# Kernel tuning notes

Measured on AMD Instinct MI355X. Metric: run time of the kernel, lower is better.

## Reference

```python
import jax, jax.numpy as jnp
import numpy as np

TOPK_RATIOS = (0.67, 0.75, 0.8)


def setup_inputs() -> dict:
    key = jax.random.key(0)
    k0, k1, k2 = jax.random.split(key, 3)
    B, L, S, H, E, D = 4, 2048, 2048, 8, 64, 64
    queries = jax.random.normal(k0, (B, L, H, E), dtype=jnp.float32)
    keys = jax.random.normal(k1, (B, S, H, E), dtype=jnp.float32)
    values = jax.random.normal(k2, (B, S, H, D), dtype=jnp.float32)
    attn_weights = jnp.ones((len(TOPK_RATIOS),), dtype=jnp.float32)  # nn.Parameter(ones)
    attn_mask = jnp.zeros((1,), dtype=bool)  # unused by the module
    return {"queries": queries, "keys": keys, "values": values,
            "attn_weights": attn_weights, "attn_mask": attn_mask}


def reference(queries, keys, values, attn_weights, attn_mask):
    # queries: [B,L,H,E], keys: [B,S,H,E], values: [B,S,H,D]
    B, L, H, E = queries.shape
    S = keys.shape[1]
    scale = 1.0 / np.sqrt(E)  # self.scale is None -> 1/sqrt(E)
    scores = jnp.einsum('blhe,bshe->bhls', queries, keys) * scale  # [B,H,L,S]
    out = jnp.zeros(queries.shape[:3] + (values.shape[-1],), dtype=scores.dtype)
    for i, ratio in enumerate(TOPK_RATIOS):
        k = int(S * ratio)
        topv = jax.lax.top_k(scores, k)[0]            # sorted descending
        kth = topv[..., -1:]                           # k-th largest per row
        # mask==0 -> -inf, then softmax over S (ties at threshold are measure-zero)
        masked = jnp.where(scores >= kth, scores, -jnp.inf)
        attn = jax.nn.softmax(masked, axis=-1)         # dropout = identity (eval)
        out = out + jnp.einsum('bhls,bshd->blhd', attn, values) * attn_weights[i]
    return out
```

## Files before the change

### kernel.cpp

```cpp
#include <hip/hip_runtime.h>
#include <hip/hip_fp16.h>

typedef _Float16 f16x8 __attribute__((ext_vector_type(8)));
typedef float f32x4 __attribute__((ext_vector_type(4)));

#define KSEL0 1372u
#define KSEL1 1536u
#define KSEL2 1638u
#define WSC 16.0f
#define QS   0.1803368801f
#define CSH2 11.5416222f

__device__ __forceinline__ unsigned ou16_inv(unsigned ou) {
  return (ou & 0x8000u) ? (ou ^ 0x8000u) : (ou ^ 0xFFFFu);
}
__device__ __forceinline__ unsigned ou16x2(unsigned uu) {
  return uu ^ 0x80008000u ^ (((uu >> 15) & 0x00010001u) * 0x7FFFu);
}
__device__ __forceinline__ unsigned pk2(float a, float b) {
  auto h = __builtin_amdgcn_cvt_pkrtz(a, b);
  return __builtin_bit_cast(unsigned, h);
}
__device__ __forceinline__ unsigned shflx(unsigned v, int m) {
  return (unsigned)__shfl_xor((int)v, m, 64);
}
__device__ __forceinline__ float h2f(unsigned bits16) {
  return __half2float(__ushort_as_half((unsigned short)bits16));
}

__device__ __forceinline__ unsigned suffix64(unsigned s4, int lane) {
  unsigned p = s4;
  #pragma unroll
  for (int off = 1; off < 64; off <<= 1) {
    int sl = lane + off;
    unsigned t = (unsigned)__shfl((int)p, sl < 64 ? sl : lane, 64);
    p += (sl < 64) ? t : 0u;
  }
  return p;
}
__device__ __forceinline__ unsigned pick_digit(unsigned tail, unsigned hx, unsigned hy,
                                               unsigned hz, unsigned hw_, unsigned k, int lane) {
  unsigned s4 = hx + hy + hz + hw_;
  unsigned a3 = tail - s4;
  unsigned a2 = a3 + hw_;
  unsigned a1 = a2 + hz;
  unsigned a0 = a1 + hy;
  int d = -1; unsigned nk = 0;
  if (a3 < k && a3 + hw_ >= k)      { d = 4*lane+3; nk = k - a3; }
  else if (a2 < k && a2 + hz >= k)  { d = 4*lane+2; nk = k - a2; }
  else if (a1 < k && a1 + hy >= k)  { d = 4*lane+1; nk = k - a1; }
  else if (a0 < k && a0 + hx >= k)  { d = 4*lane+0; nk = k - a0; }
  unsigned long long mb = __ballot(d >= 0);
  int src = __ffsll(mb) - 1;
  unsigned pack = ((unsigned)d << 16) | nk;
  return (unsigned)__shfl((int)pack, src, 64);
}

extern "C" __global__ __launch_bounds__(256)
void prep_kv(const float* __restrict__ K, const float* __restrict__ V,
             unsigned short* __restrict__ Kh, unsigned short* __restrict__ Vt) {
  if (blockIdx.x < 2048) {
    int idx = blockIdx.x * 256 + threadIdx.x;
    int ec = idx & 7;
    int s  = (idx >> 3) & 2047;
    int bh = idx >> 14;
    int b = bh >> 3, h = bh & 7;
    const float* src = K + (((size_t)b * 2048 + s) * 8 + h) * 64 + ec * 8;
    float4 a = *(const float4*)src;
    float4 c = *(const float4*)(src + 4);
    uint4 val = { pk2(a.x, a.y), pk2(a.z, a.w), pk2(c.x, c.y), pk2(c.z, c.w) };
    *(uint4*)(Kh + (size_t)idx * 8) = val;
  } else {
    const int bid  = blockIdx.x - 2048;
    const int tid  = threadIdx.x;
    const int w    = tid >> 6;
    const int lane = tid & 63;
    const int u_   = lane >> 4;
    const int dq   = (lane >> 2) & 3;
    const int r_   = lane & 3;
    const unsigned selv = (lane & 1) ? 0x03020706u : 0x05040100u;

    int bh = bid >> 4;
    int s0 = (bid & 15) * 128;
    int b = bh >> 3, h = bh & 7;
    const float* Vb = V + ((size_t)b * 2048 * 8 + h) * 64;
    unsigned short* Vo = Vt + (size_t)bh * 64 * 2048;

    #pragma unroll
    for (int sp = 0; sp < 2; ++sp) {
      #pragma unroll
      for (int p = 0; p < 4; ++p) {
        int sl = w * 32 + sp * 16 + u_ * 4;
        int sg = s0 + sl + r_;
        int d0 = p * 16 + dq * 4;
        float4 f = *(const float4*)(Vb + (size_t)sg * 512 + d0);
        unsigned lo = pk2(f.x, f.y), hi = pk2(f.z, f.w);
        unsigned tlo = shflx(lo, 1), thi = shflx(hi, 1);
        lo = __builtin_amdgcn_perm(tlo, lo, selv);
        hi = __builtin_amdgcn_perm(thi, hi, selv);
        unsigned t2lo = shflx(lo, 2), t2hi = shflx(hi, 2);
        unsigned Aw = (lane & 2) ? t2hi : lo;
        unsigned Bw = (lane & 2) ? hi   : t2lo;
        int d = d0 + r_;
        uint2 wv = {Aw, Bw};
        *(uint2*)(Vo + (size_t)d * 2048 + s0 + sl) = wv;
      }
    }
  }
}

extern "C" __global__ __launch_bounds__(512, 4)
void nma_kernel(const float* __restrict__ Q, const unsigned short* __restrict__ Kh,
                const unsigned short* __restrict__ Vt, const float* __restrict__ AW,
                float* __restrict__ Out)
{
  __shared__ __align__(16) char lds[81920];
  unsigned* work = (unsigned*)(lds + 65536);

  const int tid  = threadIdx.x;
  const int w    = tid >> 6;
  const int lane = tid & 63;
  const int g    = lane >> 4;
  const int lx   = lane & 15;

  int bid = blockIdx.x;
  int lb  = (bid & 7) * 512 + (bid >> 3);
  int bh  = lb >> 7;
  int b   = bh >> 3, hh = bh & 7;
  int l0  = (lb & 127) << 4;

  const float* Qb = Q + (((size_t)b * 2048 + l0) * 8 + hh) * 64;
  const unsigned short* Khb = Kh + (size_t)bh * 2048 * 64;
  const unsigned short* Vtb = Vt + (size_t)bh * 64 * 2048;

  {
    uint4 z4 = {0u,0u,0u,0u};
    uint4* p = (uint4*)work;
    p[tid] = z4;
    p[tid + 512] = z4;
  }

  union FU { f16x8 v; unsigned u[4]; };
  FU qa0, qa1;
  {
    const float* qp = Qb + (size_t)lx * 512 + g * 8;
    float4 a = *(const float4*)(qp);
    float4 c = *(const float4*)(qp + 4);
    qa0.u[0] = pk2(a.x*QS, a.y*QS); qa0.u[1] = pk2(a.z*QS, a.w*QS);
    qa0.u[2] = pk2(c.x*QS, c.y*QS); qa0.u[3] = pk2(c.z*QS, c.w*QS);
    a = *(const float4*)(qp + 32);
    c = *(const float4*)(qp + 36);
    qa1.u[0] = pk2(a.x*QS, a.y*QS); qa1.u[1] = pk2(a.z*QS, a.w*QS);
    qa1.u[2] = pk2(c.x*QS, c.y*QS); qa1.u[3] = pk2(c.z*QS, c.w*QS);
  }
  __syncthreads();

  const unsigned swl = ((unsigned)(lx & 7)) << 4;
  const unsigned rot = ((unsigned)lx) << 2;
  const unsigned hinc = (g < 2) ? 1u : 0x10000u;
  unsigned* hq = work + lx * 256;
  #pragma unroll 4
  for (int t = 0; t < 16; ++t) {
    int s0 = (t * 8 + w) * 16;
    const unsigned short* kp = Khb + (size_t)(s0 + lx) * 64 + g * 8;
    f16x8 kb0 = *(const f16x8*)(kp);
    f16x8 kb1 = *(const f16x8*)(kp + 32);
    f32x4 acc = {0.f, 0.f, 0.f, 0.f};
    acc = __builtin_amdgcn_mfma_f32_16x16x32_f16(kb0, qa0.v, acc, 0, 0, 0);
    acc = __builtin_amdgcn_mfma_f32_16x16x32_f16(kb1, qa1.v, acc, 0, 0, 0);
    unsigned u0 = pk2(acc[0], acc[1]);
    unsigned u1 = pk2(acc[2], acc[3]);
    uint2 wv = {u0, u1};
    *(uint2*)(lds + lx * 4096 + (((unsigned)(s0 * 2 + g * 8)) ^ swl)) = wv;
    unsigned o20 = ou16x2(u0), o21 = ou16x2(u1);
    atomicAdd(&hq[(((o20 >>  8) & 255u) + rot) & 255u], hinc);
    atomicAdd(&hq[(( o20 >> 24)         + rot) & 255u], hinc);
    atomicAdd(&hq[(((o21 >>  8) & 255u) + rot) & 255u], hinc);
    atomicAdd(&hq[(( o21 >> 24)         + rot) & 255u], hinc);
  }
  __syncthreads();

  const float aw0 = AW[0], aw1 = AW[1], aw2 = AW[2];

  unsigned d0a[2], d1a[2], d2a[2], k0a[2], k1a[2], k2a[2];
  #pragma unroll 2
  for (int rr = 0; rr < 2; ++rr) {
    int q = 2 * w + rr;
    uint4 hr = ((const uint4*)(work + q * 256))[(lane + q) & 63];
    unsigned hbx = (hr.x & 0xFFFFu) + (hr.x >> 16);
    unsigned hby = (hr.y & 0xFFFFu) + (hr.y >> 16);
    unsigned hbz = (hr.z & 0xFFFFu) + (hr.z >> 16);
    unsigned hbw = (hr.w & 0xFFFFu) + (hr.w >> 16);
    unsigned tail = suffix64(hbx + hby + hbz + hbw, lane);
    unsigned p0 = pick_digit(tail, hbx, hby, hbz, hbw, KSEL0, lane);
    unsigned p1 = pick_digit(tail, hbx, hby, hbz, hbw, KSEL1, lane);
    unsigned p2 = pick_digit(tail, hbx, hby, hbz, hbw, KSEL2, lane);
    d0a[rr] = p0 >> 16; k0a[rr] = p0 & 0xFFFFu;
    d1a[rr] = p1 >> 16; k1a[rr] = p1 & 0xFFFFu;
    d2a[rr] = p2 >> 16; k2a[rr] = p2 & 0xFFFFu;
  }

  unsigned* hw2 = work + w * 512;
  #pragma unroll 1
  for (int rr = 0; rr < 2; ++rr) {
    int q = 2 * w + rr;
    const unsigned swq = ((unsigned)(q & 7)) << 4;
    char* rowp = lds + q * 4096;
    for (int i = lane; i < 512; i += 64) hw2[i] = 0u;
    unsigned D0 = d0a[rr], D1 = d1a[rr], D2 = d2a[rr];

    unsigned ereg[16];
    #pragma unroll
    for (int it = 0; it < 4; ++it) {
      uint4 dv = *(const uint4*)(rowp + (((unsigned)(it * 1024 + lane * 16)) ^ swq));
      unsigned ws[4] = {dv.x, dv.y, dv.z, dv.w};
      #pragma unroll
      for (int p = 0; p < 4; ++p) {
        unsigned uu = ws[p];
        unsigned b0 = uu & 0xFFFFu, b1 = uu >> 16;
        unsigned o2 = ou16x2(uu);
        unsigned hi0 = (o2 >> 8) & 255u, lo0 = o2 & 255u;
        unsigned hi1 = o2 >> 24,         lo1 = (o2 >> 16) & 255u;
        unsigned add0 = (hi0 == D0 ? 1u : 0u) | (hi0 == D1 ? 0x10000u : 0u);
        unsigned add1 = (hi1 == D0 ? 1u : 0u) | (hi1 == D1 ? 0x10000u : 0u);
        if (add0) atomicAdd(&hw2[lo0], add0);
        if (hi0 == D2) atomicAdd(&hw2[256 + lo0], 1u);
        if (add1) atomicAdd(&hw2[lo1], add1);
        if (hi1 == D2) atomicAdd(&hw2[256 + lo1], 1u);
        float e0 = exp2f(h2f(b0) - CSH2);
        float e1 = exp2f(h2f(b1) - CSH2);
        ereg[it * 4 + p] = pk2(e0, e1);
      }
    }
    uint4 pkv = ((const uint4*)hw2)[lane];
    uint4 d2v = ((const uint4*)(hw2 + 256))[lane];
    unsigned ptail = suffix64(pkv.x + pkv.y + pkv.z + pkv.w, lane);
    unsigned hx = pkv.x & 0xFFFFu, hy = pkv.y & 0xFFFFu, hz = pkv.z & 0xFFFFu, hw_ = pkv.w & 0xFFFFu;
    unsigned T1o = (D0 << 8) | (pick_digit(ptail & 0xFFFFu, hx, hy, hz, hw_, k0a[rr], lane) >> 16);
    hx = pkv.x >> 16; hy = pkv.y >> 16; hz = pkv.z >> 16; hw_ = pkv.w >> 16;
    unsigned T2o = (D1 << 8) | (pick_digit(ptail >> 16, hx, hy, hz, hw_, k1a[rr], lane) >> 16);
    unsigned t2 = suffix64(d2v.x + d2v.y + d2v.z + d2v.w, lane);
    unsigned T3o = (D2 << 8) | (pick_digit(t2, d2v.x, d2v.y, d2v.z, d2v.w, k2a[rr], lane) >> 16);
    unsigned e1b = pk2(exp2f(h2f(ou16_inv(T1o)) - CSH2), 0.f) & 0xFFFFu;
    unsigned e2b = pk2(exp2f(h2f(ou16_inv(T2o)) - CSH2), 0.f) & 0xFFFFu;
    unsigned e3b = pk2(exp2f(h2f(ou16_inv(T3o)) - CSH2), 0.f) & 0xFFFFu;

    float zbA = 0.f, zbB = 0.f, zbC = 0.f;
    #pragma unroll
    for (int i = 0; i < 16; ++i) {
      unsigned uu = ereg[i];
      unsigned b0 = uu & 0xFFFFu, b1 = uu >> 16;
      float e0 = h2f(b0), e1 = h2f(b1);
      if (b0 >= e1b) zbA += e0; else if (b0 >= e2b) zbB += e0; else if (b0 >= e3b) zbC += e0;
      if (b1 >= e1b) zbA += e1; else if (b1 >= e2b) zbB += e1; else if (b1 >= e3b) zbC += e1;
    }
    #pragma unroll
    for (int off = 1; off < 64; off <<= 1) {
      zbA += __shfl_xor(zbA, off, 64);
      zbB += __shfl_xor(zbB, off, 64);
      zbC += __shfl_xor(zbC, off, 64);
    }
    float z1 = zbA, z2 = zbA + zbB, z3 = z2 + zbC;
    float A3 = aw2 / z3;
    float A2 = aw1 / z2 + A3;
    float A1 = aw0 / z1 + A2;
    unsigned A1b = pk2(A1 * WSC, 0.f) & 0xFFFFu;
    unsigned A2b = pk2(A2 * WSC, 0.f) & 0xFFFFu;
    unsigned A3b = pk2(A3 * WSC, 0.f) & 0xFFFFu;

    #pragma unroll
    for (int it = 0; it < 4; ++it) {
      unsigned no[4];
      #pragma unroll
      for (int p = 0; p < 4; ++p) {
        unsigned uu = ereg[it * 4 + p];
        unsigned b0 = uu & 0xFFFFu, b1 = uu >> 16;
        unsigned c0 = (b0 >= e1b) ? A1b : (b0 >= e2b) ? A2b : (b0 >= e3b) ? A3b : 0u;
        unsigned c1 = (b1 >= e1b) ? A1b : (b1 >= e2b) ? A2b : (b1 >= e3b) ? A3b : 0u;
        unsigned cw = c0 | (c1 << 16);
        __half2 prod = *(__half2*)&uu * *(__half2*)&cw;
        no[p] = *(unsigned*)&prod;
      }
      uint4 nv = {no[0], no[1], no[2], no[3]};
      *(uint4*)(rowp + (((unsigned)(it * 1024 + lane * 16)) ^ swq)) = nv;
    }
  }

  const int dt = (w >> 1) * 16;
  const int sh = w & 1;
  const unsigned short* vp = Vtb + (size_t)(dt + lx) * 2048 + sh * 1024 + g * 8;
  f16x8 pv0 = *(const f16x8*)(vp);
  f16x8 pv1 = *(const f16x8*)(vp + 32);
  f16x8 pv2 = *(const f16x8*)(vp + 64);
  f16x8 pv3 = *(const f16x8*)(vp + 96);
  __syncthreads();

  f32x4 oacc = {0.f, 0.f, 0.f, 0.f};
  const char* bp = lds + lx * 4096;
  const unsigned sbase = (unsigned)((sh * 1024 + g * 8) * 2);

  oacc = __builtin_amdgcn_mfma_f32_16x16x32_f16(pv0,
           *(const f16x8*)(bp + ((sbase +   0u) ^ swl)), oacc, 0, 0, 0);
  oacc = __builtin_amdgcn_mfma_f32_16x16x32_f16(pv1,
           *(const f16x8*)(bp + ((sbase +  64u) ^ swl)), oacc, 0, 0, 0);
  oacc = __builtin_amdgcn_mfma_f32_16x16x32_f16(pv2,
           *(const f16x8*)(bp + ((sbase + 128u) ^ swl)), oacc, 0, 0, 0);
  oacc = __builtin_amdgcn_mfma_f32_16x16x32_f16(pv3,
           *(const f16x8*)(bp + ((sbase + 192u) ^ swl)), oacc, 0, 0, 0);

  #pragma unroll 4
  for (int kc = 4; kc < 32; ++kc) {
    f16x8 av = *(const f16x8*)(vp + kc * 32);
    f16x8 bv = *(const f16x8*)(bp + ((sbase + (unsigned)(kc * 64)) ^ swl));
    oacc = __builtin_amdgcn_mfma_f32_16x16x32_f16(av, bv, oacc, 0, 0, 0);
  }

  float* pbuf = (float*)work;
  *(f32x4*)(pbuf + w * 256 + lx * 16 + g * 4) = oacc;
  __syncthreads();
  if (w < 4) {
    const float* pa = pbuf + (2 * w) * 256 + lx * 16 + g * 4;
    float4 ra = *(const float4*)pa;
    float4 rb = *(const float4*)(pa + 256);
    float* op = Out + (((size_t)b * 2048 + l0 + lx) * 8 + hh) * 64 + w * 16 + g * 4;
    float4 ov = { (ra.x + rb.x) * (1.f/WSC), (ra.y + rb.y) * (1.f/WSC),
                  (ra.z + rb.z) * (1.f/WSC), (ra.w + rb.w) * (1.f/WSC) };
    *(float4*)op = ov;
  }
}

extern "C" void kernel_launch(void* const* d_in, const int* in_sizes, int n_in,
                              void* d_out, int out_size, void* d_ws, size_t ws_size,
                              hipStream_t stream) {
  (void)in_sizes; (void)n_in; (void)out_size; (void)ws_size;
  const float* Q  = (const float*)d_in[0];
  const float* K  = (const float*)d_in[1];
  const float* V  = (const float*)d_in[2];
  const float* AW = (const float*)d_in[3];
  unsigned short* Kh = (unsigned short*)d_ws;
  unsigned short* Vt = (unsigned short*)((char*)d_ws + 8388608);
  prep_kv<<<dim3(2560), dim3(256), 0, stream>>>(K, V, Kh, Vt);
  nma_kernel<<<dim3(4096), dim3(512), 0, stream>>>(Q, Kh, Vt, AW, (float*)d_out);
}
```

Baseline: 350.4 us.

## Halve rows per block to shrink LDS and double grid occupancy

Each block now processes 8 query rows instead of 16, with one row per wave for the selection phase, and the grid is doubled. LDS use drops from 80KB to 48KB so more blocks can be resident per CU. Half of each 16-row MFMA tile is zero padding, so K/V loads and matrix work per output row roughly double. It also preloads more V fragments before the barrier and raises wave priority around the PV MFMA loop.

```diff
diff --git a/kernel.cpp b/kernel.cpp
--- a/kernel.cpp
+++ b/kernel.cpp
@@ -114,8 +114,8 @@
                 const unsigned short* __restrict__ Vt, const float* __restrict__ AW,
                 float* __restrict__ Out)
 {
-  __shared__ __align__(16) char lds[81920];
-  unsigned* work = (unsigned*)(lds + 65536);
+  __shared__ __align__(16) char lds[49152];
+  unsigned* work = (unsigned*)(lds + 32768);
 
   const int tid  = threadIdx.x;
   const int w    = tid >> 6;
@@ -124,10 +124,10 @@
   const int lx   = lane & 15;
 
   int bid = blockIdx.x;
-  int lb  = (bid & 7) * 512 + (bid >> 3);
-  int bh  = lb >> 7;
+  int lb  = (bid & 7) * 1024 + (bid >> 3);
+  int bh  = lb >> 8;
   int b   = bh >> 3, hh = bh & 7;
-  int l0  = (lb & 127) << 4;
+  int l0  = (lb & 255) << 3;
 
   const float* Qb = Q + (((size_t)b * 2048 + l0) * 8 + hh) * 64;
   const unsigned short* Khb = Kh + (size_t)bh * 2048 * 64;
@@ -135,14 +135,12 @@
 
   {
     uint4 z4 = {0u,0u,0u,0u};
-    uint4* p = (uint4*)work;
-    p[tid] = z4;
-    p[tid + 512] = z4;
+    ((uint4*)work)[tid] = z4;
   }
 
   union FU { f16x8 v; unsigned u[4]; };
   FU qa0, qa1;
-  {
+  if (lx < 8) {
     const float* qp = Qb + (size_t)lx * 512 + g * 8;
     float4 a = *(const float4*)(qp);
     float4 c = *(const float4*)(qp + 4);
@@ -152,13 +150,16 @@
     c = *(const float4*)(qp + 36);
     qa1.u[0] = pk2(a.x*QS, a.y*QS); qa1.u[1] = pk2(a.z*QS, a.w*QS);
     qa1.u[2] = pk2(c.x*QS, c.y*QS); qa1.u[3] = pk2(c.z*QS, c.w*QS);
+  } else {
+    qa0.u[0] = qa0.u[1] = qa0.u[2] = qa0.u[3] = 0u;
+    qa1.u[0] = qa1.u[1] = qa1.u[2] = qa1.u[3] = 0u;
   }
   __syncthreads();
 
   const unsigned swl = ((unsigned)(lx & 7)) << 4;
   const unsigned rot = ((unsigned)lx) << 2;
   const unsigned hinc = (g < 2) ? 1u : 0x10000u;
-  unsigned* hq = work + lx * 256;
+  unsigned* hq = work + (lx & 7) * 256;
   #pragma unroll 4
   for (int t = 0; t < 16; ++t) {
     int s0 = (t * 8 + w) * 16;
@@ -168,25 +169,25 @@
     f32x4 acc = {0.f, 0.f, 0.f, 0.f};
     acc = __builtin_amdgcn_mfma_f32_16x16x32_f16(kb0, qa0.v, acc, 0, 0, 0);
     acc = __builtin_amdgcn_mfma_f32_16x16x32_f16(kb1, qa1.v, acc, 0, 0, 0);
-    unsigned u0 = pk2(acc[0], acc[1]);
-    unsigned u1 = pk2(acc[2], acc[3]);
-    uint2 wv = {u0, u1};
-    *(uint2*)(lds + lx * 4096 + (((unsigned)(s0 * 2 + g * 8)) ^ swl)) = wv;
-    unsigned o20 = ou16x2(u0), o21 = ou16x2(u1);
-    atomicAdd(&hq[(((o20 >>  8) & 255u) + rot) & 255u], hinc);
-    atomicAdd(&hq[(( o20 >> 24)         + rot) & 255u], hinc);
-    atomicAdd(&hq[(((o21 >>  8) & 255u) + rot) & 255u], hinc);
-    atomicAdd(&hq[(( o21 >> 24)         + rot) & 255u], hinc);
+    if (lx < 8) {
+      unsigned u0 = pk2(acc[0], acc[1]);
+      unsigned u1 = pk2(acc[2], acc[3]);
+      uint2 wv = {u0, u1};
+      *(uint2*)(lds + lx * 4096 + (((unsigned)(s0 * 2 + g * 8)) ^ swl)) = wv;
+      unsigned o20 = ou16x2(u0), o21 = ou16x2(u1);
+      atomicAdd(&hq[(((o20 >>  8) & 255u) + rot) & 255u], hinc);
+      atomicAdd(&hq[(( o20 >> 24)         + rot) & 255u], hinc);
+      atomicAdd(&hq[(((o21 >>  8) & 255u) + rot) & 255u], hinc);
+      atomicAdd(&hq[(( o21 >> 24)         + rot) & 255u], hinc);
+    }
   }
   __syncthreads();
 
   const float aw0 = AW[0], aw1 = AW[1], aw2 = AW[2];
 
-  unsigned d0a[2], d1a[2], d2a[2], k0a[2], k1a[2], k2a[2];
-  #pragma unroll 2
-  for (int rr = 0; rr < 2; ++rr) {
-    int q = 2 * w + rr;
-    uint4 hr = ((const uint4*)(work + q * 256))[(lane + q) & 63];
+  unsigned D0, D1, D2, k0r, k1r, k2r;
+  {
+    uint4 hr = ((const uint4*)(work + w * 256))[(lane + w) & 63];
     unsigned hbx = (hr.x & 0xFFFFu) + (hr.x >> 16);
     unsigned hby = (hr.y & 0xFFFFu) + (hr.y >> 16);
     unsigned hbz = (hr.z & 0xFFFFu) + (hr.z >> 16);
@@ -195,71 +196,72 @@
     unsigned p0 = pick_digit(tail, hbx, hby, hbz, hbw, KSEL0, lane);
     unsigned p1 = pick_digit(tail, hbx, hby, hbz, hbw, KSEL1, lane);
     unsigned p2 = pick_digit(tail, hbx, hby, hbz, hbw, KSEL2, lane);
-    d0a[rr] = p0 >> 16; k0a[rr] = p0 & 0xFFFFu;
-    d1a[rr] = p1 >> 16; k1a[rr] = p1 & 0xFFFFu;
-    d2a[rr] = p2 >> 16; k2a[rr] = p2 & 0xFFFFu;
-  }
+    D0 = p0 >> 16; k0r = p0 & 0xFFFFu;
+    D1 = p1 >> 16; k1r = p1 & 0xFFFFu;
+    D2 = p2 >> 16; k2r = p2 & 0xFFFFu;
+  }
+  __syncthreads();
 
   unsigned* hw2 = work + w * 512;
-  #pragma unroll 1
-  for (int rr = 0; rr < 2; ++rr) {
-    int q = 2 * w + rr;
-    const unsigned swq = ((unsigned)(q & 7)) << 4;
-    char* rowp = lds + q * 4096;
-    for (int i = lane; i < 512; i += 64) hw2[i] = 0u;
-    unsigned D0 = d0a[rr], D1 = d1a[rr], D2 = d2a[rr];
-
-    unsigned ereg[16];
+  const unsigned swq = ((unsigned)w) << 4;
+  char* rowp = lds + w * 4096;
+  for (int i = lane; i < 512; i += 64) hw2[i] = 0u;
+
+  unsigned ereg[16];
+  #pragma unroll
+  for (int it = 0; it < 4; ++it) {
+    uint4 dv = *(const uint4*)(rowp + (((unsigned)(it * 1024 + lane * 16)) ^ swq));
+    unsigned ws[4] = {dv.x, dv.y, dv.z, dv.w};
     #pragma unroll
-    for (int it = 0; it < 4; ++it) {
-      uint4 dv = *(const uint4*)(rowp + (((unsigned)(it * 1024 + lane * 16)) ^ swq));
-      unsigned ws[4] = {dv.x, dv.y, dv.z, dv.w};
-      #pragma unroll
-      for (int p = 0; p < 4; ++p) {
-        unsigned uu = ws[p];
-        unsigned b0 = uu & 0xFFFFu, b1 = uu >> 16;
-        unsigned o2 = ou16x2(uu);
-        unsigned hi0 = (o2 >> 8) & 255u, lo0 = o2 & 255u;
-        unsigned hi1 = o2 >> 24,         lo1 = (o2 >> 16) & 255u;
-        unsigned add0 = (hi0 == D0 ? 1u : 0u) | (hi0 == D1 ? 0x10000u : 0u);
-        unsigned add1 = (hi1 == D0 ? 1u : 0u) | (hi1 == D1 ? 0x10000u : 0u);
-        if (add0) atomicAdd(&hw2[lo0], add0);
-        if (hi0 == D2) atomicAdd(&hw2[256 + lo0], 1u);
-        if (add1) atomicAdd(&hw2[lo1], add1);
-        if (hi1 == D2) atomicAdd(&hw2[256 + lo1], 1u);
-        float e0 = exp2f(h2f(b0) - CSH2);
-        float e1 = exp2f(h2f(b1) - CSH2);
-        ereg[it * 4 + p] = pk2(e0, e1);
-      }
+    for (int p = 0; p < 4; ++p) {
+      unsigned uu = ws[p];
+      unsigned b0 = uu & 0xFFFFu, b1 = uu >> 16;
+      unsigned o2 = ou16x2(uu);
+      unsigned hi0 = (o2 >> 8) & 255u, lo0 = o2 & 255u;
+      unsigned hi1 = o2 >> 24,         lo1 = (o2 >> 16) & 255u;
+      unsigned add0 = (hi0 == D0 ? 1u : 0u) | (hi0 == D1 ? 0x10000u : 0u);
+      unsigned add1 = (hi1 == D0 ? 1u : 0u) | (hi1 == D1 ? 0x10000u : 0u);
+      if (add0) atomicAdd(&hw2[lo0], add0);
+      if (hi0 == D2) atomicAdd(&hw2[256 + lo0], 1u);
+      if (add1) atomicAdd(&hw2[lo1], add1);
+      if (hi1 == D2) atomicAdd(&hw2[256 + lo1], 1u);
+      float e0 = exp2f(h2f(b0) - CSH2);
+      float e1 = exp2f(h2f(b1) - CSH2);
+      ereg[it * 4 + p] = pk2(e0, e1);
     }
+  }
+  unsigned T1o, T2o, T3o;
+  {
     uint4 pkv = ((const uint4*)hw2)[lane];
     uint4 d2v = ((const uint4*)(hw2 + 256))[lane];
     unsigned ptail = suffix64(pkv.x + pkv.y + pkv.z + pkv.w, lane);
     unsigned hx = pkv.x & 0xFFFFu, hy = pkv.y & 0xFFFFu, hz = pkv.z & 0xFFFFu, hw_ = pkv.w & 0xFFFFu;
-    unsigned T1o = (D0 << 8) | (pick_digit(ptail & 0xFFFFu, hx, hy, hz, hw_, k0a[rr], lane) >> 16);
+    T1o = (D0 << 8) | (pick_digit(ptail & 0xFFFFu, hx, hy, hz, hw_, k0r, lane) >> 16);
     hx = pkv.x >> 16; hy = pkv.y >> 16; hz = pkv.z >> 16; hw_ = pkv.w >> 16;
-    unsigned T2o = (D1 << 8) | (pick_digit(ptail >> 16, hx, hy, hz, hw_, k1a[rr], lane) >> 16);
+    T2o = (D1 << 8) | (pick_digit(ptail >> 16, hx, hy, hz, hw_, k1r, lane) >> 16);
     unsigned t2 = suffix64(d2v.x + d2v.y + d2v.z + d2v.w, lane);
-    unsigned T3o = (D2 << 8) | (pick_digit(t2, d2v.x, d2v.y, d2v.z, d2v.w, k2a[rr], lane) >> 16);
-    unsigned e1b = pk2(exp2f(h2f(ou16_inv(T1o)) - CSH2), 0.f) & 0xFFFFu;
-    unsigned e2b = pk2(exp2f(h2f(ou16_inv(T2o)) - CSH2), 0.f) & 0xFFFFu;
-    unsigned e3b = pk2(exp2f(h2f(ou16_inv(T3o)) - CSH2), 0.f) & 0xFFFFu;
-
-    float zbA = 0.f, zbB = 0.f, zbC = 0.f;
-    #pragma unroll
-    for (int i = 0; i < 16; ++i) {
-      unsigned uu = ereg[i];
-      unsigned b0 = uu & 0xFFFFu, b1 = uu >> 16;
-      float e0 = h2f(b0), e1 = h2f(b1);
-      if (b0 >= e1b) zbA += e0; else if (b0 >= e2b) zbB += e0; else if (b0 >= e3b) zbC += e0;
-      if (b1 >= e1b) zbA += e1; else if (b1 >= e2b) zbB += e1; else if (b1 >= e3b) zbC += e1;
-    }
-    #pragma unroll
-    for (int off = 1; off < 64; off <<= 1) {
-      zbA += __shfl_xor(zbA, off, 64);
-      zbB += __shfl_xor(zbB, off, 64);
-      zbC += __shfl_xor(zbC, off, 64);
-    }
+    T3o = (D2 << 8) | (pick_digit(t2, d2v.x, d2v.y, d2v.z, d2v.w, k2r, lane) >> 16);
+  }
+  unsigned e1b = pk2(exp2f(h2f(ou16_inv(T1o)) - CSH2), 0.f) & 0xFFFFu;
+  unsigned e2b = pk2(exp2f(h2f(ou16_inv(T2o)) - CSH2), 0.f) & 0xFFFFu;
+  unsigned e3b = pk2(exp2f(h2f(ou16_inv(T3o)) - CSH2), 0.f) & 0xFFFFu;
+
+  float zbA = 0.f, zbB = 0.f, zbC = 0.f;
+  #pragma unroll
+  for (int i = 0; i < 16; ++i) {
+    unsigned uu = ereg[i];
+    unsigned b0 = uu & 0xFFFFu, b1 = uu >> 16;
+    float e0 = h2f(b0), e1 = h2f(b1);
+    if (b0 >= e1b) zbA += e0; else if (b0 >= e2b) zbB += e0; else if (b0 >= e3b) zbC += e0;
+    if (b1 >= e1b) zbA += e1; else if (b1 >= e2b) zbB += e1; else if (b1 >= e3b) zbC += e1;
+  }
+  #pragma unroll
+  for (int off = 1; off < 64; off <<= 1) {
+    zbA += __shfl_xor(zbA, off, 64);
+    zbB += __shfl_xor(zbB, off, 64);
+    zbC += __shfl_xor(zbC, off, 64);
+  }
+  {
     float z1 = zbA, z2 = zbA + zbB, z3 = z2 + zbC;
     float A3 = aw2 / z3;
     float A2 = aw1 / z2 + A3;
@@ -293,12 +295,17 @@
   f16x8 pv1 = *(const f16x8*)(vp + 32);
   f16x8 pv2 = *(const f16x8*)(vp + 64);
   f16x8 pv3 = *(const f16x8*)(vp + 96);
+  f16x8 pv4 = *(const f16x8*)(vp + 128);
+  f16x8 pv5 = *(const f16x8*)(vp + 160);
+  f16x8 pv6 = *(const f16x8*)(vp + 192);
+  f16x8 pv7 = *(const f16x8*)(vp + 224);
   __syncthreads();
 
   f32x4 oacc = {0.f, 0.f, 0.f, 0.f};
-  const char* bp = lds + lx * 4096;
+  const char* bp = lds + (lx & 7) * 4096;
   const unsigned sbase = (unsigned)((sh * 1024 + g * 8) * 2);
 
+  __builtin_amdgcn_s_setprio(1);
   oacc = __builtin_amdgcn_mfma_f32_16x16x32_f16(pv0,
            *(const f16x8*)(bp + ((sbase +   0u) ^ swl)), oacc, 0, 0, 0);
   oacc = __builtin_amdgcn_mfma_f32_16x16x32_f16(pv1,
@@ -307,18 +314,27 @@
            *(const f16x8*)(bp + ((sbase + 128u) ^ swl)), oacc, 0, 0, 0);
   oacc = __builtin_amdgcn_mfma_f32_16x16x32_f16(pv3,
            *(const f16x8*)(bp + ((sbase + 192u) ^ swl)), oacc, 0, 0, 0);
+  oacc = __builtin_amdgcn_mfma_f32_16x16x32_f16(pv4,
+           *(const f16x8*)(bp + ((sbase + 256u) ^ swl)), oacc, 0, 0, 0);
+  oacc = __builtin_amdgcn_mfma_f32_16x16x32_f16(pv5,
+           *(const f16x8*)(bp + ((sbase + 320u) ^ swl)), oacc, 0, 0, 0);
+  oacc = __builtin_amdgcn_mfma_f32_16x16x32_f16(pv6,
+           *(const f16x8*)(bp + ((sbase + 384u) ^ swl)), oacc, 0, 0, 0);
+  oacc = __builtin_amdgcn_mfma_f32_16x16x32_f16(pv7,
+           *(const f16x8*)(bp + ((sbase + 448u) ^ swl)), oacc, 0, 0, 0);
 
   #pragma unroll 4
-  for (int kc = 4; kc < 32; ++kc) {
+  for (int kc = 8; kc < 32; ++kc) {
     f16x8 av = *(const f16x8*)(vp + kc * 32);
     f16x8 bv = *(const f16x8*)(bp + ((sbase + (unsigned)(kc * 64)) ^ swl));
     oacc = __builtin_amdgcn_mfma_f32_16x16x32_f16(av, bv, oacc, 0, 0, 0);
   }
+  __builtin_amdgcn_s_setprio(0);
 
   float* pbuf = (float*)work;
   *(f32x4*)(pbuf + w * 256 + lx * 16 + g * 4) = oacc;
   __syncthreads();
-  if (w < 4) {
+  if (w < 4 && lx < 8) {
     const float* pa = pbuf + (2 * w) * 256 + lx * 16 + g * 4;
     float4 ra = *(const float4*)pa;
     float4 rb = *(const float4*)(pa + 256);
@@ -340,5 +356,5 @@
   unsigned short* Kh = (unsigned short*)d_ws;
   unsigned short* Vt = (unsigned short*)((char*)d_ws + 8388608);
   prep_kv<<<dim3(2560), dim3(256), 0, stream>>>(K, V, Kh, Vt);
-  nma_kernel<<<dim3(4096), dim3(512), 0, stream>>>(Q, Kh, Vt, AW, (float*)d_out);
-}
+  nma_kernel<<<dim3(8192), dim3(512), 0, stream>>>(Q, Kh, Vt, AW, (float*)d_out);
+}
```

Result: slower. 512.1 us (+46.2%).
